# Optimization experiments

Hardware: AMD Instinct MI355X
Metric: run time of the kernel (lower is better)

## Reference

```python
import jax, jax.numpy as jnp
import numpy as np

N, E, F, H, C = 50000, 800000, 602, 32, 41
BN_EPS = 1e-5


def _mlp(h, Wa, ba, Wb, bb):
    return jax.nn.relu(h @ Wa + ba) @ Wb + bb


def _bn(h, gamma, beta):
    # BatchNorm1d training mode: per-feature batch mean / biased variance
    m = jnp.mean(h, axis=0)
    v = jnp.var(h, axis=0)
    return (h - m) * jax.lax.rsqrt(v + BN_EPS) * gamma + beta


def _gin(x, row, col, Wa, ba, Wb, bb):
    # sum-aggregate neighbor features (SpMM via gather + segment_sum), eps=0
    agg = jax.ops.segment_sum(x[col], row, num_segments=x.shape[0])
    return _mlp(x + agg, Wa, ba, Wb, bb)


def setup_inputs() -> dict:
    key = jax.random.key(0)
    ks = jax.random.split(key, 16)
    s = 0.05
    inp = {
        "x": jax.random.normal(ks[0], (N, F), dtype=jnp.float32),
        "row": jax.random.randint(ks[1], (E,), 0, N),
        "col": jax.random.randint(ks[2], (E,), 0, N),
        # conv1 MLP
        "W1a": jax.random.normal(ks[3], (F, H), dtype=jnp.float32) * s,
        "b1a": jnp.zeros((H,), jnp.float32),
        "W1b": jax.random.normal(ks[4], (H, H), dtype=jnp.float32) * s,
        "b1b": jnp.zeros((H,), jnp.float32),
        "g1": jnp.ones((H,), jnp.float32),
        "be1": jnp.zeros((H,), jnp.float32),
        # conv2 MLP
        "W2a": jax.random.normal(ks[5], (H, H), dtype=jnp.float32) * s,
        "b2a": jnp.zeros((H,), jnp.float32),
        "W2b": jax.random.normal(ks[6], (H, H), dtype=jnp.float32) * s,
        "b2b": jnp.zeros((H,), jnp.float32),
        "g2": jnp.ones((H,), jnp.float32),
        "be2": jnp.zeros((H,), jnp.float32),
        # heads
        "Wf1": jax.random.normal(ks[7], (H, H), dtype=jnp.float32) * s,
        "bf1": jnp.zeros((H,), jnp.float32),
        "Wf2": jax.random.normal(ks[8], (H, C), dtype=jnp.float32) * s,
        "bf2": jnp.zeros((C,), jnp.float32),
    }
    return inp


def reference(x, row, col, W1a, b1a, W1b, b1b, g1, be1,
              W2a, b2a, W2b, b2b, g2, be2, Wf1, bf1, Wf2, bf2):
    h = _bn(_gin(x, row, col, W1a, b1a, W1b, b1b), g1, be1)
    h = _bn(_gin(h, row, col, W2a, b2a, W2b, b2b), g2, be2)
    h = jax.nn.relu(h @ Wf1 + bf1)
    return h @ Wf2 + bf2
```

## Files before the change

### kernel.cpp

```cpp
#include <hip/hip_runtime.h>
#include <hip/hip_bf16.h>

#define N_NODES 50000
#define F_IN    602
#define H_DIM   32
#define C_OUT   41
#define E_EDGES 800000
#define BN_EPS  1e-5f

__global__ __launch_bounds__(256) void k_gemm_in(
    const float* __restrict__ x, const float* __restrict__ W,
    const float* __restrict__ b, float* __restrict__ p, float* __restrict__ z) {
  __shared__ float xs[128 * 36];
  __shared__ float ws[32 * 36];
  const int tid = threadIdx.x;
  const int cg = tid & 7;
  const int rgg = tid >> 3;
  const int r0 = blockIdx.x * 128;

  float acc[4][4] = {};

  for (int k0 = 0; k0 < F_IN; k0 += 32) {
    const int kc = min(32, F_IN - k0);
    for (int i = 0; i < 8; i++) {
      int f = tid + 256 * i;
      int r = f >> 4;
      int kh = (f & 15) << 1;
      float2 v = {0.f, 0.f};
      int gr = r0 + r;
      if (gr < N_NODES) {
        int k = k0 + kh;
        if (k + 2 <= F_IN) v = *(const float2*)(x + (size_t)gr * F_IN + k);
        else if (k < F_IN) v.x = x[(size_t)gr * F_IN + k];
      }
      *(float2*)&xs[r * 36 + kh] = v;
    }
    for (int i = 0; i < 4; i++) {
      int f = tid + 256 * i;
      int k = f >> 5, c = f & 31;
      ws[c * 36 + k] = (k < kc) ? W[(size_t)(k0 + k) * H_DIM + c] : 0.f;
    }
    __syncthreads();
    #pragma unroll
    for (int kq = 0; kq < 8; kq++) {
      float4 xv[4], wv[4];
      #pragma unroll
      for (int i = 0; i < 4; i++) xv[i] = *(float4*)&xs[(rgg + 32 * i) * 36 + kq * 4];
      #pragma unroll
      for (int j = 0; j < 4; j++) wv[j] = *(float4*)&ws[(cg + 8 * j) * 36 + kq * 4];
      #pragma unroll
      for (int i = 0; i < 4; i++)
        #pragma unroll
        for (int j = 0; j < 4; j++)
          acc[i][j] += xv[i].x * wv[j].x + xv[i].y * wv[j].y +
                       xv[i].z * wv[j].z + xv[i].w * wv[j].w;
    }
    __syncthreads();
  }

  #pragma unroll
  for (int i = 0; i < 4; i++) {
    int gr = r0 + rgg + 32 * i;
    if (gr < N_NODES) {
      #pragma unroll
      for (int j = 0; j < 4; j++) {
        int c = cg + 8 * j;
        float v = acc[i][j];
        p[(size_t)gr * H_DIM + c] = v;
        z[(size_t)gr * H_DIM + c] = v + b[c];
      }
    }
  }
}

__global__ __launch_bounds__(256) void k_scatter(
    const int* __restrict__ row, const int* __restrict__ col,
    const float* __restrict__ p, float* __restrict__ z) {
  long long t = (long long)blockIdx.x * 256 + threadIdx.x;
  int e = (int)(t >> 5);
  int c = (int)(t & 31);
  if (e < E_EDGES) {
    int s = col[e], d = row[e];
    atomicAdd(&z[(size_t)d * H_DIM + c], p[(size_t)s * H_DIM + c]);
  }
}

__global__ __launch_bounds__(256) void k_mlp_stats(
    const float* __restrict__ z, const float* __restrict__ W,
    const float* __restrict__ b, float* __restrict__ hpre,
    float* __restrict__ stats) {
  __shared__ float as_[64 * 36];
  __shared__ float ws[32 * 36];
  __shared__ float red[512];
  const int tid = threadIdx.x;
  for (int i = tid; i < 1024; i += 256) {
    int k = i >> 5, c = i & 31;
    ws[c * 36 + k] = W[(size_t)k * H_DIM + c];
  }
  const int r0 = blockIdx.x * 64;
  for (int i = tid; i < 2048; i += 256) {
    int r = i >> 5, c = i & 31;
    int gr = r0 + r;
    float v = (gr < N_NODES) ? z[(size_t)gr * H_DIM + c] : 0.f;
    as_[r * 36 + c] = fmaxf(v, 0.f);
  }
  __syncthreads();
  const int c = tid & 31, rg = tid >> 5;
  float4 wc[8];
  #pragma unroll
  for (int q = 0; q < 8; q++) wc[q] = *(float4*)&ws[c * 36 + q * 4];
  const float bc = b[c];
  float lsum = 0.f, lsq = 0.f;
  #pragma unroll
  for (int i = 0; i < 8; i++) {
    int r = rg * 8 + i;
    float a = bc;
    #pragma unroll
    for (int q = 0; q < 8; q++) {
      float4 h4 = *(float4*)&as_[r * 36 + q * 4];
      a += h4.x * wc[q].x + h4.y * wc[q].y + h4.z * wc[q].z + h4.w * wc[q].w;
    }
    int gr = r0 + r;
    if (gr < N_NODES) {
      hpre[(size_t)gr * H_DIM + c] = a;
      lsum += a; lsq += a * a;
    }
  }
  __syncthreads();
  red[tid] = lsum; red[256 + tid] = lsq;
  __syncthreads();
  if (tid < 32) {
    float s = 0.f, q = 0.f;
    #pragma unroll
    for (int g = 0; g < 8; g++) { s += red[g * 32 + tid]; q += red[256 + g * 32 + tid]; }
    atomicAdd(&stats[tid], s);
    atomicAdd(&stats[32 + tid], q);
  }
}

__global__ void k_bnfin(const float* __restrict__ stats, const float* __restrict__ g,
                        const float* __restrict__ be, float* __restrict__ ss) {
  int c = threadIdx.x;
  if (c < H_DIM) {
    float m = stats[c] / (float)N_NODES;
    float v = stats[32 + c] / (float)N_NODES - m * m;
    float sc = g[c] * rsqrtf(v + BN_EPS);
    ss[c] = sc;
    ss[32 + c] = be[c] - m * sc;
  }
}

__global__ __launch_bounds__(256) void k_gemm32_affine(
    const float* __restrict__ hpre, const float* __restrict__ ss,
    const float* __restrict__ W, const float* __restrict__ bz,
    float* __restrict__ p, float* __restrict__ z) {
  __shared__ float hs[64 * 36];
  __shared__ float ws[32 * 36];
  const int tid = threadIdx.x;
  for (int i = tid; i < 1024; i += 256) {
    int k = i >> 5, c = i & 31;
    ws[c * 36 + k] = W[(size_t)k * H_DIM + c];
  }
  const int r0 = blockIdx.x * 64;
  for (int i = tid; i < 2048; i += 256) {
    int r = i >> 5, c = i & 31;
    int gr = r0 + r;
    float v = (gr < N_NODES) ? hpre[(size_t)gr * H_DIM + c] * ss[c] + ss[32 + c] : 0.f;
    hs[r * 36 + c] = v;
  }
  __syncthreads();
  const int c = tid & 31, rg = tid >> 5;
  float4 wc[8];
  #pragma unroll
  for (int q = 0; q < 8; q++) wc[q] = *(float4*)&ws[c * 36 + q * 4];
  const float bzc = bz[c];
  #pragma unroll
  for (int i = 0; i < 8; i++) {
    int r = rg * 8 + i;
    float a = 0.f;
    #pragma unroll
    for (int q = 0; q < 8; q++) {
      float4 h4 = *(float4*)&hs[r * 36 + q * 4];
      a += h4.x * wc[q].x + h4.y * wc[q].y + h4.z * wc[q].z + h4.w * wc[q].w;
    }
    int gr = r0 + r;
    if (gr < N_NODES) {
      p[(size_t)gr * H_DIM + c] = a;
      z[(size_t)gr * H_DIM + c] = a + bzc;
    }
  }
}

__global__ __launch_bounds__(256) void k_heads(
    const float* __restrict__ hpre, const float* __restrict__ ss,
    const float* __restrict__ W1, const float* __restrict__ b1,
    const float* __restrict__ W2, const float* __restrict__ b2,
    float* __restrict__ out) {
  __shared__ float hs[64 * 36];
  __shared__ float fs[64 * 36];
  __shared__ float w1[32 * 36];
  __shared__ float w2[41 * 36];
  const int tid = threadIdx.x;
  for (int i = tid; i < 1024; i += 256) {
    int k = i >> 5, c = i & 31;
    w1[c * 36 + k] = W1[(size_t)k * H_DIM + c];
  }
  for (int i = tid; i < 41 * 32; i += 256) {
    int j = i >> 5, k = i & 31;
    w2[j * 36 + k] = W2[(size_t)k * C_OUT + j];
  }
  const int r0 = blockIdx.x * 64;
  for (int i = tid; i < 2048; i += 256) {
    int r = i >> 5, c = i & 31;
    int gr = r0 + r;
    hs[r * 36 + c] = (gr < N_NODES) ? hpre[(size_t)gr * H_DIM + c] * ss[c] + ss[32 + c] : 0.f;
  }
  __syncthreads();
  {
    const int c = tid & 31, rg = tid >> 5;
    float4 wc[8];
    #pragma unroll
    for (int q = 0; q < 8; q++) wc[q] = *(float4*)&w1[c * 36 + q * 4];
    const float bc = b1[c];
    #pragma unroll
    for (int i = 0; i < 8; i++) {
      int r = rg * 8 + i;
      float a = bc;
      #pragma unroll
      for (int q = 0; q < 8; q++) {
        float4 h4 = *(float4*)&hs[r * 36 + q * 4];
        a += h4.x * wc[q].x + h4.y * wc[q].y + h4.z * wc[q].z + h4.w * wc[q].w;
      }
      fs[r * 36 + c] = fmaxf(a, 0.f);
    }
  }
  __syncthreads();
  for (int idx = tid; idx < 64 * C_OUT; idx += 256) {
    int r = idx / C_OUT, j = idx - r * C_OUT;
    int gr = r0 + r;
    if (gr < N_NODES) {
      float a = b2[j];
      #pragma unroll
      for (int q = 0; q < 8; q++) {
        float4 f4 = *(float4*)&fs[r * 36 + q * 4];
        float4 w4 = *(float4*)&w2[j * 36 + q * 4];
        a += f4.x * w4.x + f4.y * w4.y + f4.z * w4.z + f4.w * w4.w;
      }
      out[(size_t)gr * C_OUT + j] = a;
    }
  }
}

extern "C" void kernel_launch(void* const* d_in, const int* in_sizes, int n_in,
                              void* d_out, int out_size, void* d_ws, size_t ws_size,
                              hipStream_t stream) {
  const float* x   = (const float*)d_in[0];
  const int* row   = (const int*)d_in[1];
  const int* col   = (const int*)d_in[2];
  const float* W1a = (const float*)d_in[3];
  const float* b1a = (const float*)d_in[4];
  const float* W1b = (const float*)d_in[5];
  const float* b1b = (const float*)d_in[6];
  const float* g1  = (const float*)d_in[7];
  const float* be1 = (const float*)d_in[8];
  const float* W2a = (const float*)d_in[9];
  const float* b2a = (const float*)d_in[10];
  const float* W2b = (const float*)d_in[11];
  const float* b2b = (const float*)d_in[12];
  const float* g2  = (const float*)d_in[13];
  const float* be2 = (const float*)d_in[14];
  const float* Wf1 = (const float*)d_in[15];
  const float* bf1 = (const float*)d_in[16];
  const float* Wf2 = (const float*)d_in[17];
  const float* bf2 = (const float*)d_in[18];
  float* out = (float*)d_out;

  float* ws = (float*)d_ws;
  float* pA    = ws;
  float* zB    = ws + (size_t)N_NODES * H_DIM;
  float* hC    = ws + (size_t)2 * N_NODES * H_DIM;
  float* stats = ws + (size_t)3 * N_NODES * H_DIM;

  hipMemsetAsync(stats, 0, 256 * sizeof(float), stream);

  const int gBig   = (N_NODES + 127) / 128;
  const int g64    = (N_NODES + 63) / 64;
  const int gScat  = (E_EDGES * 32 + 255) / 256;

  k_gemm_in<<<gBig, 256, 0, stream>>>(x, W1a, b1a, pA, zB);
  k_scatter<<<gScat, 256, 0, stream>>>(row, col, pA, zB);
  k_mlp_stats<<<g64, 256, 0, stream>>>(zB, W1b, b1b, hC, stats);
  k_bnfin<<<1, 64, 0, stream>>>(stats, g1, be1, stats + 64);
  k_gemm32_affine<<<g64, 256, 0, stream>>>(hC, stats + 64, W2a, b2a, pA, zB);
  k_scatter<<<gScat, 256, 0, stream>>>(row, col, pA, zB);
  k_mlp_stats<<<g64, 256, 0, stream>>>(zB, W2b, b2b, hC, stats + 128);
  k_bnfin<<<1, 64, 0, stream>>>(stats + 128, g2, be2, stats + 192);
  k_heads<<<g64, 256, 0, stream>>>(hC, stats + 192, Wf1, bf1, Wf2, bf2, out);
}
```

Before: 567.4 us.

## Build CSR per call and replace atomic scatter with gather aggregation; restructure input GEMM

Builds a CSR adjacency on the device each call (degree histogram, three-stage scan, atomic fill) and replaces the per-edge atomicAdd scatter with a per-node gather that sums neighbor rows into a register and writes once, with the bias folded in. The input GEMM is rewritten to stage the whole weight matrix in shared memory as float4 in two phases while streaming x rows directly from global memory, with each block handling two row groups. The aim is to remove atomic contention on the 800k edges across two aggregation passes. The cost is the extra CSR build kernels per call, nondeterministic neighbor order within each row, and a fallback path when workspace is too small.

```diff
diff --git a/kernel.cpp b/kernel.cpp
--- a/kernel.cpp
+++ b/kernel.cpp
@@ -8,69 +8,170 @@
 #define E_EDGES 800000
 #define BN_EPS  1e-5f
 
-__global__ __launch_bounds__(256) void k_gemm_in(
+#define GEMM_GRID 1024
+
+__global__ __launch_bounds__(256) void k_gemm_in_v2(
     const float* __restrict__ x, const float* __restrict__ W,
-    const float* __restrict__ b, float* __restrict__ p, float* __restrict__ z) {
-  __shared__ float xs[128 * 36];
-  __shared__ float ws[32 * 36];
+    float* __restrict__ p) {
+  __shared__ float4 wq[76 * 32];
   const int tid = threadIdx.x;
-  const int cg = tid & 7;
-  const int rgg = tid >> 3;
-  const int r0 = blockIdx.x * 128;
-
-  float acc[4][4] = {};
-
-  for (int k0 = 0; k0 < F_IN; k0 += 32) {
-    const int kc = min(32, F_IN - k0);
-    for (int i = 0; i < 8; i++) {
-      int f = tid + 256 * i;
-      int r = f >> 4;
-      int kh = (f & 15) << 1;
-      float2 v = {0.f, 0.f};
-      int gr = r0 + r;
-      if (gr < N_NODES) {
-        int k = k0 + kh;
-        if (k + 2 <= F_IN) v = *(const float2*)(x + (size_t)gr * F_IN + k);
-        else if (k < F_IN) v.x = x[(size_t)gr * F_IN + k];
+  const int w = tid >> 6;
+  const int l = tid & 63;
+  const int h = l >> 5;
+  const int c = l & 31;
+
+  const int g0 = blockIdx.x;
+  const int g1 = blockIdx.x + GEMM_GRID;
+  const bool has1 = (g1 * 32 < N_NODES);
+  int rb[2] = { g0 * 32 + w * 8 + h * 4, g1 * 32 + w * 8 + h * 4 };
+
+  float acc[2][4] = {};
+
+  for (int ph = 0; ph < 2; ph++) {
+    const int qbase = ph ? 76 : 0;
+    const int nq    = ph ? 75 : 76;
+    if (ph) __syncthreads();
+    for (int i = tid; i < nq * 32; i += 256) {
+      int q = i >> 5, cc = i & 31;
+      int k4 = (qbase + q) * 4;
+      float4 v;
+      v.x = W[(size_t)k4 * H_DIM + cc];
+      v.y = (k4 + 1 < F_IN) ? W[(size_t)(k4 + 1) * H_DIM + cc] : 0.f;
+      v.z = (k4 + 2 < F_IN) ? W[(size_t)(k4 + 2) * H_DIM + cc] : 0.f;
+      v.w = (k4 + 3 < F_IN) ? W[(size_t)(k4 + 3) * H_DIM + cc] : 0.f;
+      wq[q * 32 + cc] = v;
+    }
+    __syncthreads();
+
+    for (int gi = 0; gi < 2; gi++) {
+      if (gi && !has1) break;
+      const int r0 = rb[gi];
+      const float* xr[4];
+      #pragma unroll
+      for (int i = 0; i < 4; i++) {
+        int rr = r0 + i; if (rr > N_NODES - 1) rr = N_NODES - 1;
+        xr[i] = x + (size_t)rr * F_IN;
       }
-      *(float2*)&xs[r * 36 + kh] = v;
-    }
+      #pragma unroll 2
+      for (int q = 0; q < nq; q++) {
+        float4 w4 = wq[q * 32 + c];
+        const int k = (qbase + q) * 4;
+        const bool tail = (qbase + q) == 150;
+        #pragma unroll
+        for (int i = 0; i < 4; i++) {
+          float2 a = *(const float2*)(xr[i] + k);
+          float2 bv;
+          if (tail) { bv.x = 0.f; bv.y = 0.f; }
+          else      { bv = *(const float2*)(xr[i] + k + 2); }
+          acc[gi][i] += a.x * w4.x + a.y * w4.y + bv.x * w4.z + bv.y * w4.w;
+        }
+      }
+    }
+  }
+
+  #pragma unroll
+  for (int gi = 0; gi < 2; gi++) {
+    if (gi && !has1) break;
+    const int r0 = rb[gi];
+    #pragma unroll
     for (int i = 0; i < 4; i++) {
-      int f = tid + 256 * i;
-      int k = f >> 5, c = f & 31;
-      ws[c * 36 + k] = (k < kc) ? W[(size_t)(k0 + k) * H_DIM + c] : 0.f;
-    }
+      int rr = r0 + i;
+      if (rr < N_NODES) p[(size_t)rr * H_DIM + c] = acc[gi][i];
+    }
+  }
+}
+
+__global__ __launch_bounds__(256) void k_hist(const int* __restrict__ row,
+                                              int* __restrict__ deg) {
+  int e = blockIdx.x * 256 + threadIdx.x;
+  if (e < E_EDGES) atomicAdd(&deg[row[e]], 1);
+}
+
+__global__ __launch_bounds__(256) void k_scanA(const int* __restrict__ deg,
+                                               int* __restrict__ start,
+                                               int* __restrict__ bsum) {
+  __shared__ int sc[256];
+  int t = threadIdx.x, i = blockIdx.x * 256 + t;
+  int v = (i < N_NODES) ? deg[i] : 0;
+  sc[t] = v;
+  __syncthreads();
+  #pragma unroll
+  for (int off = 1; off < 256; off <<= 1) {
+    int u = (t >= off) ? sc[t - off] : 0;
     __syncthreads();
-    #pragma unroll
-    for (int kq = 0; kq < 8; kq++) {
-      float4 xv[4], wv[4];
-      #pragma unroll
-      for (int i = 0; i < 4; i++) xv[i] = *(float4*)&xs[(rgg + 32 * i) * 36 + kq * 4];
-      #pragma unroll
-      for (int j = 0; j < 4; j++) wv[j] = *(float4*)&ws[(cg + 8 * j) * 36 + kq * 4];
-      #pragma unroll
-      for (int i = 0; i < 4; i++)
-        #pragma unroll
-        for (int j = 0; j < 4; j++)
-          acc[i][j] += xv[i].x * wv[j].x + xv[i].y * wv[j].y +
-                       xv[i].z * wv[j].z + xv[i].w * wv[j].w;
-    }
+    sc[t] += u;
     __syncthreads();
   }
-
-  #pragma unroll
-  for (int i = 0; i < 4; i++) {
-    int gr = r0 + rgg + 32 * i;
-    if (gr < N_NODES) {
-      #pragma unroll
-      for (int j = 0; j < 4; j++) {
-        int c = cg + 8 * j;
-        float v = acc[i][j];
-        p[(size_t)gr * H_DIM + c] = v;
-        z[(size_t)gr * H_DIM + c] = v + b[c];
-      }
-    }
-  }
+  if (i < N_NODES) start[i] = sc[t] - v;
+  if (t == 255) bsum[blockIdx.x] = sc[255];
+}
+
+__global__ __launch_bounds__(256) void k_scanB(const int* __restrict__ bsum,
+                                               int* __restrict__ boff, int nb) {
+  __shared__ int sc[256];
+  int t = threadIdx.x;
+  int v = (t < nb) ? bsum[t] : 0;
+  sc[t] = v;
+  __syncthreads();
+  #pragma unroll
+  for (int off = 1; off < 256; off <<= 1) {
+    int u = (t >= off) ? sc[t - off] : 0;
+    __syncthreads();
+    sc[t] += u;
+    __syncthreads();
+  }
+  if (t < nb) boff[t] = sc[t] - v;
+}
+
+__global__ __launch_bounds__(256) void k_scanC(int* __restrict__ start,
+                                               const int* __restrict__ boff,
+                                               int* __restrict__ cursor) {
+  int i = blockIdx.x * 256 + threadIdx.x;
+  if (i < N_NODES) {
+    int s = start[i] + boff[blockIdx.x];
+    start[i] = s;
+    cursor[i] = s;
+  }
+  if (i == 0) start[N_NODES] = E_EDGES;
+}
+
+__global__ __launch_bounds__(256) void k_fill(const int* __restrict__ row,
+                                              const int* __restrict__ col,
+                                              int* __restrict__ cursor,
+                                              int* __restrict__ ecol) {
+  int e = blockIdx.x * 256 + threadIdx.x;
+  if (e < E_EDGES) {
+    int pos = atomicAdd(&cursor[row[e]], 1);
+    ecol[pos] = col[e];
+  }
+}
+
+__global__ __launch_bounds__(256) void k_gather(
+    const float* __restrict__ p, const float* __restrict__ b,
+    const int* __restrict__ start, const int* __restrict__ ecol,
+    float* __restrict__ z) {
+  int hw = (blockIdx.x * 256 + threadIdx.x) >> 5;
+  int c = threadIdx.x & 31;
+  if (hw >= N_NODES) return;
+  int s = start[hw], e = start[hw + 1];
+  float acc = p[(size_t)hw * H_DIM + c] + b[c];
+  int i = s;
+  for (; i + 1 < e; i += 2) {
+    int s0 = ecol[i], s1 = ecol[i + 1];
+    float v0 = p[(size_t)s0 * H_DIM + c];
+    float v1 = p[(size_t)s1 * H_DIM + c];
+    acc += v0;
+    acc += v1;
+  }
+  if (i < e) acc += p[(size_t)ecol[i] * H_DIM + c];
+  z[(size_t)hw * H_DIM + c] = acc;
+}
+
+__global__ __launch_bounds__(256) void k_zinit(const float* __restrict__ p,
+                                               const float* __restrict__ b,
+                                               float* __restrict__ z) {
+  int i = blockIdx.x * 256 + threadIdx.x;
+  if (i < N_NODES * H_DIM) z[i] = p[i] + b[i & 31];
 }
 
 __global__ __launch_bounds__(256) void k_scatter(
@@ -152,8 +253,7 @@
 
 __global__ __launch_bounds__(256) void k_gemm32_affine(
     const float* __restrict__ hpre, const float* __restrict__ ss,
-    const float* __restrict__ W, const float* __restrict__ bz,
-    float* __restrict__ p, float* __restrict__ z) {
+    const float* __restrict__ W, float* __restrict__ p) {
   __shared__ float hs[64 * 36];
   __shared__ float ws[32 * 36];
   const int tid = threadIdx.x;
@@ -173,7 +273,6 @@
   float4 wc[8];
   #pragma unroll
   for (int q = 0; q < 8; q++) wc[q] = *(float4*)&ws[c * 36 + q * 4];
-  const float bzc = bz[c];
   #pragma unroll
   for (int i = 0; i < 8; i++) {
     int r = rg * 8 + i;
@@ -184,10 +283,7 @@
       a += h4.x * wc[q].x + h4.y * wc[q].y + h4.z * wc[q].z + h4.w * wc[q].w;
     }
     int gr = r0 + r;
-    if (gr < N_NODES) {
-      p[(size_t)gr * H_DIM + c] = a;
-      z[(size_t)gr * H_DIM + c] = a + bzc;
-    }
+    if (gr < N_NODES) p[(size_t)gr * H_DIM + c] = a;
   }
 }
 
@@ -276,23 +372,53 @@
   float* out = (float*)d_out;
 
   float* ws = (float*)d_ws;
+  const size_t NH = (size_t)N_NODES * H_DIM;
   float* pA    = ws;
-  float* zB    = ws + (size_t)N_NODES * H_DIM;
-  float* hC    = ws + (size_t)2 * N_NODES * H_DIM;
-  float* stats = ws + (size_t)3 * N_NODES * H_DIM;
+  float* zB    = ws + NH;
+  float* hC    = ws + 2 * NH;
+  float* stats = ws + 3 * NH;
+  int*   startA = (int*)(ws + 3 * NH + 256);
+  int*   cursor = startA + 50016;
+  int*   deg    = cursor + 50016;
+  int*   ecol   = deg + 50016;
+  int*   bsum   = ecol + E_EDGES;
+  int*   boff   = bsum + 256;
+  const size_t need_bytes = ((3 * NH + 256) + 3 * 50016 + E_EDGES + 512) * 4;
+  const bool use_csr = (ws_size >= need_bytes);
 
   hipMemsetAsync(stats, 0, 256 * sizeof(float), stream);
 
-  const int gBig   = (N_NODES + 127) / 128;
-  const int g64    = (N_NODES + 63) / 64;
-  const int gScat  = (E_EDGES * 32 + 255) / 256;
-
-  k_gemm_in<<<gBig, 256, 0, stream>>>(x, W1a, b1a, pA, zB);
-  k_scatter<<<gScat, 256, 0, stream>>>(row, col, pA, zB);
+  const int g64   = (N_NODES + 63) / 64;
+  const int gE    = (E_EDGES + 255) / 256;
+  const int gN    = (N_NODES + 255) / 256;
+  const int gHW   = (N_NODES * 32 + 255) / 256;
+  const int gScat = (E_EDGES * 32 + 255) / 256;
+
+  if (use_csr) {
+    hipMemsetAsync(deg, 0, 50000 * sizeof(int), stream);
+    k_hist <<<gE, 256, 0, stream>>>(row, deg);
+    k_scanA<<<gN, 256, 0, stream>>>(deg, startA, bsum);
+    k_scanB<<<1, 256, 0, stream>>>(bsum, boff, gN);
+    k_scanC<<<gN, 256, 0, stream>>>(startA, boff, cursor);
+    k_fill <<<gE, 256, 0, stream>>>(row, col, cursor, ecol);
+  }
+
+  k_gemm_in_v2<<<GEMM_GRID, 256, 0, stream>>>(x, W1a, pA);
+  if (use_csr) {
+    k_gather<<<gHW, 256, 0, stream>>>(pA, b1a, startA, ecol, zB);
+  } else {
+    k_zinit<<<g64 * 8, 256, 0, stream>>>(pA, b1a, zB);
+    k_scatter<<<gScat, 256, 0, stream>>>(row, col, pA, zB);
+  }
   k_mlp_stats<<<g64, 256, 0, stream>>>(zB, W1b, b1b, hC, stats);
   k_bnfin<<<1, 64, 0, stream>>>(stats, g1, be1, stats + 64);
-  k_gemm32_affine<<<g64, 256, 0, stream>>>(hC, stats + 64, W2a, b2a, pA, zB);
-  k_scatter<<<gScat, 256, 0, stream>>>(row, col, pA, zB);
+  k_gemm32_affine<<<g64, 256, 0, stream>>>(hC, stats + 64, W2a, pA);
+  if (use_csr) {
+    k_gather<<<gHW, 256, 0, stream>>>(pA, b2a, startA, ecol, zB);
+  } else {
+    k_zinit<<<g64 * 8, 256, 0, stream>>>(pA, b2a, zB);
+    k_scatter<<<gScat, 256, 0, stream>>>(row, col, pA, zB);
+  }
   k_mlp_stats<<<g64, 256, 0, stream>>>(zB, W2b, b2b, hC, stats + 128);
   k_bnfin<<<1, 64, 0, stream>>>(stats + 128, g2, be2, stats + 192);
   k_heads<<<g64, 256, 0, stream>>>(hC, stats + 192, Wf1, bf1, Wf2, bf2, out);
```

Measured after the change: 629.3 us. 1.11x slower.
